# Performance work log

Measured on AMD Instinct MI355X. Metric: run time of the kernel, lower is better.

The kernel has to match this reference:

```python
import jax, jax.numpy as jnp
import numpy as np

N = 50000   # nodes
E = 800000  # edges (avg degree 16)
D = 128     # emb_dim
K = 3       # message passing rounds


def setup_inputs() -> dict:
    key = jax.random.key(0)
    ks = jax.random.split(key, 24)
    scale = jnp.float32(0.1)  # keep k iterated MLP magnitudes sane

    def w(k, shape):
        return jax.random.normal(k, shape, dtype=jnp.float32) * scale

    inp = {
        "feat": jax.random.normal(ks[0], (N, D), dtype=jnp.float32),
        "src": jax.random.randint(ks[1], (E,), 0, N, dtype=jnp.int32),
        "dst": jax.random.randint(ks[2], (E,), 0, N, dtype=jnp.int32),
    }
    i = 3
    for name in ["nt", "fp", "fu", "bp", "bu"]:
        inp[name + "_w1"] = w(ks[i], (D, D))
        inp[name + "_b1"] = w(ks[i + 1], (D,))
        inp[name + "_w2"] = w(ks[i + 2], (D, D))
        inp[name + "_b2"] = w(ks[i + 3], (D,))
        i += 4
    return inp


def _fnn(x, w1, b1, w2, b2):
    # FNN(in,[hid],out): Linear -> ReLU -> Linear (no final activation)
    return jnp.maximum(x @ w1 + b1, 0.0) @ w2 + b2


def _aggregate(y, src, dst, pw1, pb1, pw2, pb2, uw1, ub1, uw2, ub2):
    # gather src node states -> edge MLP (+ReLU) -> scatter-sum -> node MLP (+ReLU)
    msg = jnp.maximum(_fnn(y[src], pw1, pb1, pw2, pb2), 0.0)   # [E, D]
    z = jax.ops.segment_sum(msg, dst, num_segments=N)          # [N, D]
    return jnp.maximum(_fnn(z, uw1, ub1, uw2, ub2), 0.0)       # [N, D]


def _message_pass(self_trans, src, dst, sink, params):
    y = self_trans
    for _ in range(K):
        h = _aggregate(y, src, dst, *params)
        h = h.at[sink].set(0.0)  # zero the sink node row
        y = self_trans + h
    return y


def reference(feat, src, dst,
              nt_w1, nt_b1, nt_w2, nt_b2,
              fp_w1, fp_b1, fp_w2, fp_b2,
              fu_w1, fu_b1, fu_w2, fu_b2,
              bp_w1, bp_b1, bp_w2, bp_b2,
              bu_w1, bu_b1, bu_w2, bu_b2):
    self_trans = _fnn(feat, nt_w1, nt_b1, nt_w2, nt_b2)  # [N, D]
    # forward-direction aggregator, sink = last node
    out_fpa = _message_pass(self_trans, src, dst, N - 1,
                            (fp_w1, fp_b1, fp_w2, fp_b2,
                             fu_w1, fu_b1, fu_w2, fu_b2))
    # reversed graph (dgl.reverse swaps src/dst), sink = node 0
    out_bpa = _message_pass(self_trans, dst, src, 0,
                            (bp_w1, bp_b1, bp_w2, bp_b2,
                             bu_w1, bu_b1, bu_w2, bu_b2))
    return jnp.concatenate([out_fpa, out_bpa], axis=1)  # [N, 2D]
```

## Files before the change

### kernel.cpp

```cpp
#include <hip/hip_runtime.h>

#define Nn 50000
#define Ee 800000
#define Dd 128
#define Kk 3
#define TE 64
#define NT 256

#define LSTR 136
#define WSLOT 32768

#define NBUK 196
#define SCH 2048
#define SB ((Ee + SCH - 1) / SCH)

typedef short sh8 __attribute__((ext_vector_type(8)));
typedef float f32x4 __attribute__((ext_vector_type(4)));

__device__ __forceinline__ ushort bfsplit(float x, float* rem) {
  const unsigned u = __float_as_uint(x);
  *rem = x - __uint_as_float(u & 0xffff0000u);
  return (ushort)(u >> 16);
}
__device__ __forceinline__ ushort bftrunc(float x) {
  return (ushort)(__float_as_uint(x) >> 16);
}
__device__ __forceinline__ ushort f32_to_bf16_rtn(float x) {
  const unsigned u = __float_as_uint(x);
  return (ushort)((u + 0x7fffu + ((u >> 16) & 1u)) >> 16);
}

__device__ __forceinline__ void acc8(const uint4 v, float4& a0, float4& a1) {
  a0.x += __uint_as_float(v.x << 16);
  a0.y += __uint_as_float(v.x & 0xffff0000u);
  a0.z += __uint_as_float(v.y << 16);
  a0.w += __uint_as_float(v.y & 0xffff0000u);
  a1.x += __uint_as_float(v.z << 16);
  a1.y += __uint_as_float(v.z & 0xffff0000u);
  a1.z += __uint_as_float(v.w << 16);
  a1.w += __uint_as_float(v.w & 0xffff0000u);
}

#define MFMA_LAYER(WH, WL)                                                     \
  {                                                                            \
    _Pragma("unroll")                                                          \
    for (int c = 0; c < 4; ++c) {                                              \
      const sh8 bh0 = *(const sh8*)((WH) + (((nt0    ) * 4 + c) * 64 + lane) * 8); \
      const sh8 bh1 = *(const sh8*)((WH) + (((nt0 + 1) * 4 + c) * 64 + lane) * 8); \
      const sh8 bl0 = *(const sh8*)((WL) + (((nt0    ) * 4 + c) * 64 + lane) * 8); \
      const sh8 bl1 = *(const sh8*)((WL) + (((nt0 + 1) * 4 + c) * 64 + lane) * 8); \
      _Pragma("unroll")                                                        \
      for (int mt = 0; mt < 4; ++mt) {                                         \
        const int aoff = (mt * 16 + l15) * LSTR + c * 32 + q8 * 8;             \
        const sh8 ah = *(const sh8*)(Sh + aoff);                               \
        const sh8 al = *(const sh8*)(Sl + aoff);                               \
        acc[mt][0] = __builtin_amdgcn_mfma_f32_16x16x32_bf16(ah, bh0, acc[mt][0], 0, 0, 0); \
        acc[mt][1] = __builtin_amdgcn_mfma_f32_16x16x32_bf16(ah, bh1, acc[mt][1], 0, 0, 0); \
        acc[mt][0] = __builtin_amdgcn_mfma_f32_16x16x32_bf16(al, bh0, acc[mt][0], 0, 0, 0); \
        acc[mt][1] = __builtin_amdgcn_mfma_f32_16x16x32_bf16(al, bh1, acc[mt][1], 0, 0, 0); \
        acc[mt][0] = __builtin_amdgcn_mfma_f32_16x16x32_bf16(ah, bl0, acc[mt][0], 0, 0, 0); \
        acc[mt][1] = __builtin_amdgcn_mfma_f32_16x16x32_bf16(ah, bl1, acc[mt][1], 0, 0, 0); \
      }                                                                        \
    }                                                                          \
  }

#define ZERO_ACC                                                 \
  {                                                              \
    _Pragma("unroll")                                            \
    for (int mt = 0; mt < 4; ++mt)                               \
      _Pragma("unroll")                                          \
      for (int nl = 0; nl < 2; ++nl) {                           \
        acc[mt][nl][0] = 0.f; acc[mt][nl][1] = 0.f;              \
        acc[mt][nl][2] = 0.f; acc[mt][nl][3] = 0.f;              \
      }                                                          \
  }

#define HIDDEN_TO_LDS(B1ptr)                                     \
  {                                                              \
    const float b1a = (B1ptr)[w32 + l15];                        \
    const float b1b = (B1ptr)[w32 + 16 + l15];                   \
    _Pragma("unroll")                                            \
    for (int mt = 0; mt < 4; ++mt)                               \
      _Pragma("unroll")                                          \
      for (int nl = 0; nl < 2; ++nl) {                           \
        const int col = w32 + nl * 16 + l15;                     \
        const float bb = nl ? b1b : b1a;                         \
        _Pragma("unroll")                                        \
        for (int rg = 0; rg < 4; ++rg) {                         \
          const int row = mt * 16 + q8 * 4 + rg;                 \
          const float h = fmaxf(acc[mt][nl][rg] + bb, 0.f);      \
          float rm;                                              \
          const ushort hh = bfsplit(h, &rm);                     \
          const int off = row * LSTR + col;                      \
          Sh[off] = hh;                                          \
          Sl[off] = bftrunc(rm);                                 \
        }                                                        \
      }                                                          \
  }

#define STC_TO_LDS                                               \
  {                                                              \
    _Pragma("unroll")                                            \
    for (int mt = 0; mt < 4; ++mt)                               \
      _Pragma("unroll")                                          \
      for (int nl = 0; nl < 2; ++nl) {                           \
        const int col = w32 + nl * 16 + l15;                     \
        _Pragma("unroll")                                        \
        for (int rg = 0; rg < 4; ++rg) {                         \
          const int row = mt * 16 + q8 * 4 + rg;                 \
          float rm;                                              \
          const ushort hh = bfsplit(stc[mt][nl][rg], &rm);       \
          const int off = row * LSTR + col;                      \
          Sh[off] = hh;                                          \
          Sl[off] = bftrunc(rm);                                 \
        }                                                        \
      }                                                          \
  }

#define STAGE_ROWS(Xptr)                                                       \
  {                                                                            \
    _Pragma("unroll")                                                          \
    for (int it = 0; it < (TE * 32 / NT); ++it) {                              \
      const int i = t + NT * it;                                               \
      const int r = i >> 5;                                                    \
      const int c4 = (i & 31) << 2;                                            \
      float4 v = make_float4(0.f, 0.f, 0.f, 0.f);                              \
      if (r < nrow) v = *(const float4*)((Xptr) + (size_t)(row0 + r) * Dd + c4); \
      ushort4 hv, lv; float rm;                                                \
      hv.x = bfsplit(v.x, &rm); lv.x = bftrunc(rm);                            \
      hv.y = bfsplit(v.y, &rm); lv.y = bftrunc(rm);                            \
      hv.z = bfsplit(v.z, &rm); lv.z = bftrunc(rm);                            \
      hv.w = bfsplit(v.w, &rm); lv.w = bftrunc(rm);                            \
      *(ushort4*)(&Sh[r * LSTR + c4]) = hv;                                    \
      *(ushort4*)(&Sl[r * LSTR + c4]) = lv;                                    \
    }                                                                          \
  }

#define MFMA_PRELUDE                                             \
  const int lane = t & 63;                                       \
  const int wave = t >> 6;                                       \
  const int l15 = lane & 15;                                     \
  const int q8 = lane >> 4;                                      \
  const int w32 = wave * 32;                                     \
  const int nt0 = wave * 2;                                      \
  f32x4 acc[4][2];

struct DirP {
  const ushort *u1, *u2, *p1, *p2;
  const float *ub1, *ub2, *pb1, *pb2;
};

__global__ __launch_bounds__(NT) void stmsg_kernel(
    const float* __restrict__ X,
    const ushort* __restrict__ Wn1, const ushort* __restrict__ Wn2,
    const float* __restrict__ Bn1, const float* __restrict__ Bn2,
    DirP pf, DirP pb,
    float* __restrict__ st, ushort* __restrict__ Mf, ushort* __restrict__ Mb)
{
  __shared__ __align__(16) ushort Sbuf[2 * TE * LSTR];
  ushort* Sh = Sbuf;
  ushort* Sl = Sbuf + TE * LSTR;
  const int t = threadIdx.x;
  const int row0 = blockIdx.x * TE;
  const int rem = Nn - row0;
  const int nrow = rem < TE ? rem : TE;

  STAGE_ROWS(X);
  __syncthreads();
  MFMA_PRELUDE;

  ZERO_ACC;
  MFMA_LAYER(Wn1, Wn1 + 16384);
  __syncthreads();
  HIDDEN_TO_LDS(Bn1);
  __syncthreads();
  ZERO_ACC;
  MFMA_LAYER(Wn2, Wn2 + 16384);

  float stc[4][2][4];
  {
    const float b2a = Bn2[w32 + l15];
    const float b2b = Bn2[w32 + 16 + l15];
    #pragma unroll
    for (int mt = 0; mt < 4; ++mt)
      #pragma unroll
      for (int nl = 0; nl < 2; ++nl) {
        const int col = w32 + nl * 16 + l15;
        const float bb = nl ? b2b : b2a;
        #pragma unroll
        for (int rg = 0; rg < 4; ++rg) {
          const int row = mt * 16 + q8 * 4 + rg;
          const float v = acc[mt][nl][rg] + bb;
          stc[mt][nl][rg] = v;
          if (row < nrow) st[(size_t)(row0 + row) * Dd + col] = v;
        }
      }
  }
  __syncthreads();

  STC_TO_LDS;
  __syncthreads();
  ZERO_ACC;
  MFMA_LAYER(pf.p1, pf.p1 + 16384);
  __syncthreads();
  HIDDEN_TO_LDS(pf.pb1);
  __syncthreads();
  ZERO_ACC;
  MFMA_LAYER(pf.p2, pf.p2 + 16384);
  {
    const float b2a = pf.pb2[w32 + l15];
    const float b2b = pf.pb2[w32 + 16 + l15];
    #pragma unroll
    for (int mt = 0; mt < 4; ++mt)
      #pragma unroll
      for (int nl = 0; nl < 2; ++nl) {
        const int col = w32 + nl * 16 + l15;
        const float bb = nl ? b2b : b2a;
        #pragma unroll
        for (int rg = 0; rg < 4; ++rg) {
          const int row = mt * 16 + q8 * 4 + rg;
          if (row < nrow)
            Mf[(size_t)(row0 + row) * Dd + col] =
                f32_to_bf16_rtn(fmaxf(acc[mt][nl][rg] + bb, 0.f));
        }
      }
  }
  __syncthreads();

  STC_TO_LDS;
  __syncthreads();
  ZERO_ACC;
  MFMA_LAYER(pb.p1, pb.p1 + 16384);
  __syncthreads();
  HIDDEN_TO_LDS(pb.pb1);
  __syncthreads();
  ZERO_ACC;
  MFMA_LAYER(pb.p2, pb.p2 + 16384);
  {
    const float b2a = pb.pb2[w32 + l15];
    const float b2b = pb.pb2[w32 + 16 + l15];
    #pragma unroll
    for (int mt = 0; mt < 4; ++mt)
      #pragma unroll
      for (int nl = 0; nl < 2; ++nl) {
        const int col = w32 + nl * 16 + l15;
        const float bb = nl ? b2b : b2a;
        #pragma unroll
        for (int rg = 0; rg < 4; ++rg) {
          const int row = mt * 16 + q8 * 4 + rg;
          if (row < nrow)
            Mb[(size_t)(row0 + row) * Dd + col] =
                f32_to_bf16_rtn(fmaxf(acc[mt][nl][rg] + bb, 0.f));
        }
      }
  }
}

template <int DO_MSG>
__global__ __launch_bounds__(NT) void aggupdmsg_kernel(
    const ushort* __restrict__ Min_f, const ushort* __restrict__ Min_b,
    const int* __restrict__ rp_f, const int* __restrict__ rp_b,
    const int* __restrict__ col_f, const int* __restrict__ col_b,
    const float* __restrict__ st,
    ushort* __restrict__ RMf, ushort* __restrict__ RMb,
    float* __restrict__ RYf, float* __restrict__ RYb, int rstride,
    DirP pf, DirP pb, int nhalf)
{
  __shared__ __align__(16) ushort Sbuf[2 * TE * LSTR];
  ushort* Sh = Sbuf;
  ushort* Sl = Sbuf + TE * LSTR;
  const int t = threadIdx.x;
  const int dir = blockIdx.x >= nhalf;
  const int row0 = (blockIdx.x - dir * nhalf) * TE;
  const int rem = Nn - row0;
  const int nrow = rem < TE ? rem : TE;
  const DirP P = dir ? pb : pf;
  const ushort* Min = dir ? Min_b : Min_f;
  const int* rp = dir ? rp_b : rp_f;
  const int* col = dir ? col_b : col_f;
  ushort* RoutM = dir ? RMb : RMf;
  float* RoutY = dir ? RYb : RYf;
  const int sink = dir ? 0 : (Nn - 1);

  {
    const int nr = t >> 2;
    const int q4 = t & 3;
    const int qb = (t & 63) & 60;
    float4 za[8];
    #pragma unroll
    for (int i = 0; i < 8; ++i) za[i] = make_float4(0.f, 0.f, 0.f, 0.f);
    if (nr < nrow) {
      const int gnode = row0 + nr;
      int e = rp[gnode];
      const int ee = rp[gnode + 1];
      const ushort* Mq4 = Min + q4 * 8;
      for (; e + 3 < ee; e += 4) {
        const int cm = col[e + q4];
        const int c0 = __shfl(cm, qb);
        const int c1 = __shfl(cm, qb + 1);
        const int c2 = __shfl(cm, qb + 2);
        const int c3 = __shfl(cm, qb + 3);
        const ushort* r0 = Mq4 + (size_t)c0 * Dd;
        const ushort* r1 = Mq4 + (size_t)c1 * Dd;
        const ushort* r2 = Mq4 + (size_t)c2 * Dd;
        const ushort* r3 = Mq4 + (size_t)c3 * Dd;
        uint4 v0[4], v1[4], v2[4], v3[4];
        #pragma unroll
        for (int i = 0; i < 4; ++i) v0[i] = *(const uint4*)(r0 + i * 32);
        #pragma unroll
        for (int i = 0; i < 4; ++i) v1[i] = *(const uint4*)(r1 + i * 32);
        #pragma unroll
        for (int i = 0; i < 4; ++i) v2[i] = *(const uint4*)(r2 + i * 32);
        #pragma unroll
        for (int i = 0; i < 4; ++i) v3[i] = *(const uint4*)(r3 + i * 32);
        #pragma unroll
        for (int i = 0; i < 4; ++i) {
          acc8(v0[i], za[2 * i], za[2 * i + 1]);
          acc8(v1[i], za[2 * i], za[2 * i + 1]);
          acc8(v2[i], za[2 * i], za[2 * i + 1]);
          acc8(v3[i], za[2 * i], za[2 * i + 1]);
        }
      }
      for (; e < ee; ++e) {
        const ushort* r0 = Mq4 + (size_t)col[e] * Dd;
        #pragma unroll
        for (int i = 0; i < 4; ++i)
          acc8(*(const uint4*)(r0 + i * 32), za[2 * i], za[2 * i + 1]);
      }
    }
    #pragma unroll
    for (int k = 0; k < 8; ++k) {
      ushort4 hv, lv; float rm;
      hv.x = bfsplit(za[k].x, &rm); lv.x = bftrunc(rm);
      hv.y = bfsplit(za[k].y, &rm); lv.y = bftrunc(rm);
      hv.z = bfsplit(za[k].z, &rm); lv.z = bftrunc(rm);
      hv.w = bfsplit(za[k].w, &rm); lv.w = bftrunc(rm);
      const int c4 = (k >> 1) * 32 + q4 * 8 + (k & 1) * 4;
      *(ushort4*)(&Sh[nr * LSTR + c4]) = hv;
      *(ushort4*)(&Sl[nr * LSTR + c4]) = lv;
    }
  }
  __syncthreads();

  MFMA_PRELUDE;

  ZERO_ACC;
  MFMA_LAYER(P.u1, P.u1 + 16384);
  __syncthreads();
  HIDDEN_TO_LDS(P.ub1);
  __syncthreads();
  ZERO_ACC;
  MFMA_LAYER(P.u2, P.u2 + 16384);

  {
    const float b2a = P.ub2[w32 + l15];
    const float b2b = P.ub2[w32 + 16 + l15];
    if (DO_MSG) __syncthreads();
    #pragma unroll
    for (int mt = 0; mt < 4; ++mt)
      #pragma unroll
      for (int nl = 0; nl < 2; ++nl) {
        const int col = w32 + nl * 16 + l15;
        const float bb = nl ? b2b : b2a;
        #pragma unroll
        for (int rg = 0; rg < 4; ++rg) {
          const int row = mt * 16 + q8 * 4 + rg;
          float v = 0.f;
          if (row < nrow) {
            const int gr = row0 + row;
            v = fmaxf(acc[mt][nl][rg] + bb, 0.f);
            if (gr == sink) v = 0.f;
            v += st[(size_t)gr * Dd + col];
          }
          if (DO_MSG) {
            float rm;
            const ushort hh = bfsplit(v, &rm);
            const int off = row * LSTR + col;
            Sh[off] = hh;
            Sl[off] = bftrunc(rm);
          } else if (row < nrow) {
            RoutY[(size_t)(row0 + row) * rstride + col] = v;
          }
        }
      }
  }

  if (DO_MSG) {
    __syncthreads();
    ZERO_ACC;
    MFMA_LAYER(P.p1, P.p1 + 16384);
    __syncthreads();
    HIDDEN_TO_LDS(P.pb1);
    __syncthreads();
    ZERO_ACC;
    MFMA_LAYER(P.p2, P.p2 + 16384);

    const float b2a = P.pb2[w32 + l15];
    const float b2b = P.pb2[w32 + 16 + l15];
    #pragma unroll
    for (int mt = 0; mt < 4; ++mt)
      #pragma unroll
      for (int nl = 0; nl < 2; ++nl) {
        const int col = w32 + nl * 16 + l15;
        const float bb = nl ? b2b : b2a;
        #pragma unroll
        for (int rg = 0; rg < 4; ++rg) {
          const int row = mt * 16 + q8 * 4 + rg;
          if (row < nrow)
            RoutM[(size_t)(row0 + row) * Dd + col] =
                f32_to_bf16_rtn(fmaxf(acc[mt][nl][rg] + bb, 0.f));
        }
      }
  }
}

struct WPtrs { const float* w[10]; };

__global__ void pack_w_kernel(WPtrs P, ushort* __restrict__ out)
{
  const int id = blockIdx.x * blockDim.x + threadIdx.x;
  const int mat = blockIdx.y;
  const int j = id & 7;
  const int lane = (id >> 3) & 63;
  const int ch = (id >> 9) & 3;
  const int nt = id >> 11;
  const int k = ch * 32 + (lane >> 4) * 8 + j;
  const int n = nt * 16 + (lane & 15);
  const float x = P.w[mat][k * Dd + n];
  float rm;
  const ushort h = bfsplit(x, &rm);
  out[(size_t)mat * WSLOT + id] = h;
  out[(size_t)mat * WSLOT + 16384 + id] = bftrunc(rm);
}

__global__ __launch_bounds__(256) void csr_count(
    const int* __restrict__ src, const int* __restrict__ dst,
    int* __restrict__ bcnt)
{
  const int dirv = blockIdx.y;
  const int* key = dirv ? src : dst;
  __shared__ int h[NBUK];
  const int t = threadIdx.x;
  if (t < NBUK) h[t] = 0;
  __syncthreads();
  const int e0 = blockIdx.x * SCH;
  #pragma unroll
  for (int i = 0; i < SCH / 256; ++i) {
    const int e = e0 + i * 256 + t;
    if (e < Ee) atomicAdd(&h[key[e] >> 8], 1);
  }
  __syncthreads();
  if (t < NBUK && h[t] > 0) atomicAdd(&bcnt[dirv * 256 + t], h[t]);
}

__global__ __launch_bounds__(256) void csr_scan(
    const int* __restrict__ bcnt, int* __restrict__ bbase,
    int* __restrict__ bcur, int* __restrict__ rp)
{
  __shared__ int s[256];
  const int t = threadIdx.x;
  for (int y = 0; y < 2; ++y) {
    const int v = (t < NBUK) ? bcnt[y * 256 + t] : 0;
    s[t] = v;
    __syncthreads();
    for (int off = 1; off < 256; off <<= 1) {
      int x = s[t];
      if (t >= off) x += s[t - off];
      __syncthreads();
      s[t] = x;
      __syncthreads();
    }
    const int excl = s[t] - v;
    if (t < NBUK) { bbase[y * 257 + t] = excl; bcur[y * 256 + t] = excl; }
    if (t == NBUK - 1) bbase[y * 257 + NBUK] = s[t];
    if (t == 0) rp[y * (Nn + 1) + Nn] = Ee;
    __syncthreads();
  }
}

__global__ __launch_bounds__(256) void csr_scatter(
    const int* __restrict__ src, const int* __restrict__ dst,
    int* __restrict__ bcur, uint* __restrict__ pairs)
{
  const int dirv = blockIdx.y;
  const int* key = dirv ? src : dst;
  const int* val = dirv ? dst : src;
  __shared__ int lh[NBUK], gb[NBUK], lc[NBUK];
  const int t = threadIdx.x;
  if (t < NBUK) { lh[t] = 0; lc[t] = 0; }
  __syncthreads();
  const int e0 = blockIdx.x * SCH;
  int ks[SCH / 256], vs[SCH / 256];
  #pragma unroll
  for (int i = 0; i < SCH / 256; ++i) {
    const int e = e0 + i * 256 + t;
    ks[i] = (e < Ee) ? key[e] : -1;
    vs[i] = (e < Ee) ? val[e] : 0;
    if (ks[i] >= 0) atomicAdd(&lh[ks[i] >> 8], 1);
  }
  __syncthreads();
  if (t < NBUK && lh[t] > 0) gb[t] = atomicAdd(&bcur[dirv * 256 + t], lh[t]);
  __syncthreads();
  uint* pd = pairs + (size_t)dirv * Ee;
  #pragma unroll
  for (int i = 0; i < SCH / 256; ++i) {
    if (ks[i] >= 0) {
      const int b = ks[i] >> 8;
      const int r = atomicAdd(&lc[b], 1);
      pd[gb[b] + r] = ((uint)ks[i] << 16) | (uint)vs[i];
    }
  }
}

__global__ __launch_bounds__(256) void csr_final(
    const uint* __restrict__ pairs, const int* __restrict__ bbase,
    int* __restrict__ rp, int* __restrict__ col_f, int* __restrict__ col_b)
{
  const int dirv = blockIdx.y;
  const int b = blockIdx.x;
  const int base = bbase[dirv * 257 + b];
  const int cnt = bbase[dirv * 257 + b + 1] - base;
  const uint* pd = pairs + (size_t)dirv * Ee + base;
  int* colo = dirv ? col_b : col_f;
  __shared__ int h[256];
  __shared__ int s[256];
  const int t = threadIdx.x;
  h[t] = 0;
  __syncthreads();
  for (int i = t; i < cnt; i += 256) atomicAdd(&h[(pd[i] >> 16) & 255], 1);
  __syncthreads();
  const int v = h[t];
  s[t] = v;
  __syncthreads();
  for (int off = 1; off < 256; off <<= 1) {
    int x = s[t];
    if (t >= off) x += s[t - off];
    __syncthreads();
    s[t] = x;
    __syncthreads();
  }
  const int excl = s[t] - v;
  const int node = b * 256 + t;
  if (node < Nn) rp[dirv * (Nn + 1) + node] = base + excl;
  h[t] = excl;
  __syncthreads();
  for (int i = t; i < cnt; i += 256) {
    const uint p = pd[i];
    const int k = (p >> 16) & 255;
    const int r = atomicAdd(&h[k], 1);
    colo[base + r] = (int)(p & 0xffffu);
  }
}

extern "C" void kernel_launch(void* const* d_in, const int* in_sizes, int n_in,
                              void* d_out, int out_size, void* d_ws, size_t ws_size,
                              hipStream_t stream)
{
  const float* feat = (const float*)d_in[0];
  const int*   src  = (const int*)d_in[1];
  const int*   dst  = (const int*)d_in[2];

  const float* W[5][4];
  for (int p = 0; p < 5; ++p)
    for (int q = 0; q < 4; ++q)
      W[p][q] = (const float*)d_in[3 + p * 4 + q];

  float* st = (float*)d_ws;
  ushort* Mp_f = (ushort*)(st + (size_t)Nn * Dd);
  ushort* Mp_b = Mp_f + (size_t)Nn * Dd;
  ushort* Mq_f = Mp_b + (size_t)Nn * Dd;
  ushort* Mq_b = Mq_f + (size_t)Nn * Dd;
  int* ip       = (int*)(Mq_b + (size_t)Nn * Dd);
  int* rp_f     = ip;                 ip += Nn + 1;
  int* rp_b     = ip;                 ip += Nn + 1;
  int* col_f    = ip;                 ip += Ee;
  int* col_b    = ip;                 ip += Ee;
  int* bcnt     = ip;                 ip += 2 * 256;
  int* bbase    = ip;                 ip += 2 * 257;
  int* bcur     = ip;                 ip += 2 * 256;
  ushort* Wp = (ushort*)(((uintptr_t)ip + 63) & ~(uintptr_t)63);
  float* out = (float*)d_out;

  uint* pairs = (uint*)Mq_f;

  const int nodeBlocks = (Nn + TE - 1) / TE;
  const int dualBlocks = 2 * nodeBlocks;

  WPtrs wpk;
  for (int p = 0; p < 5; ++p) { wpk.w[2 * p] = W[p][0]; wpk.w[2 * p + 1] = W[p][2]; }
  pack_w_kernel<<<dim3(64, 10), NT, 0, stream>>>(wpk, Wp);

  hipMemsetAsync(bcnt, 0, 2 * 256 * sizeof(int), stream);
  csr_count<<<dim3(SB, 2), 256, 0, stream>>>(src, dst, bcnt);
  csr_scan<<<1, 256, 0, stream>>>(bcnt, bbase, bcur, rp_f);
  csr_scatter<<<dim3(SB, 2), 256, 0, stream>>>(src, dst, bcur, pairs);
  csr_final<<<dim3(NBUK, 2), 256, 0, stream>>>(pairs, bbase, rp_f, col_f, col_b);

  #define WS(m) (Wp + (size_t)(m) * WSLOT)
  DirP Pf = { WS(4), WS(5), WS(2), WS(3), W[2][1], W[2][3], W[1][1], W[1][3] };
  DirP Pb = { WS(8), WS(9), WS(6), WS(7), W[4][1], W[4][3], W[3][1], W[3][3] };

  stmsg_kernel<<<nodeBlocks, NT, 0, stream>>>(
      feat, WS(0), WS(1), W[0][1], W[0][3], Pf, Pb, st, Mp_f, Mp_b);

  aggupdmsg_kernel<1><<<dualBlocks, NT, 0, stream>>>(
      Mp_f, Mp_b, rp_f, rp_b, col_f, col_b, st,
      Mq_f, Mq_b, nullptr, nullptr, 0, Pf, Pb, nodeBlocks);

  aggupdmsg_kernel<1><<<dualBlocks, NT, 0, stream>>>(
      Mq_f, Mq_b, rp_f, rp_b, col_f, col_b, st,
      Mp_f, Mp_b, nullptr, nullptr, 0, Pf, Pb, nodeBlocks);

  aggupdmsg_kernel<0><<<dualBlocks, NT, 0, stream>>>(
      Mp_f, Mp_b, rp_f, rp_b, col_f, col_b, st,
      nullptr, nullptr, out, out + Dd, 2 * Dd, Pf, Pb, nodeBlocks);

  #undef WS
}
```

Baseline: 582.8 us.

## Double block threads to 512, one 16-col MFMA tile per wave, 8-lane gather

Raises the thread count per block from 256 to 512, so each of 8 waves computes one 16-column output tile in the MFMA layers instead of two, halving per-wave accumulator registers. The neighbor gather is reorganized so 8 lanes cooperate per node, each loading 16 bytes from two halves of a row, and 8 edges are unrolled per iteration instead of 4. This aims at more memory-level parallelism and occupancy for the gather-bound aggregation. In exchange, each block carries more waves across its syncs, and the A-tile LDS reads are now repeated by more waves.

```diff
diff --git a/kernel.cpp b/kernel.cpp
--- a/kernel.cpp
+++ b/kernel.cpp
@@ -6,6 +6,7 @@
 #define Kk 3
 #define TE 64
 #define NT 256
+#define NTM 512
 
 #define LSTR 136
 #define WSLOT 32768
@@ -45,21 +46,16 @@
   {                                                                            \
     _Pragma("unroll")                                                          \
     for (int c = 0; c < 4; ++c) {                                              \
-      const sh8 bh0 = *(const sh8*)((WH) + (((nt0    ) * 4 + c) * 64 + lane) * 8); \
-      const sh8 bh1 = *(const sh8*)((WH) + (((nt0 + 1) * 4 + c) * 64 + lane) * 8); \
-      const sh8 bl0 = *(const sh8*)((WL) + (((nt0    ) * 4 + c) * 64 + lane) * 8); \
-      const sh8 bl1 = *(const sh8*)((WL) + (((nt0 + 1) * 4 + c) * 64 + lane) * 8); \
+      const sh8 bh = *(const sh8*)((WH) + ((wave * 4 + c) * 64 + lane) * 8);   \
+      const sh8 bl = *(const sh8*)((WL) + ((wave * 4 + c) * 64 + lane) * 8);   \
       _Pragma("unroll")                                                        \
       for (int mt = 0; mt < 4; ++mt) {                                         \
         const int aoff = (mt * 16 + l15) * LSTR + c * 32 + q8 * 8;             \
         const sh8 ah = *(const sh8*)(Sh + aoff);                               \
         const sh8 al = *(const sh8*)(Sl + aoff);                               \
-        acc[mt][0] = __builtin_amdgcn_mfma_f32_16x16x32_bf16(ah, bh0, acc[mt][0], 0, 0, 0); \
-        acc[mt][1] = __builtin_amdgcn_mfma_f32_16x16x32_bf16(ah, bh1, acc[mt][1], 0, 0, 0); \
-        acc[mt][0] = __builtin_amdgcn_mfma_f32_16x16x32_bf16(al, bh0, acc[mt][0], 0, 0, 0); \
-        acc[mt][1] = __builtin_amdgcn_mfma_f32_16x16x32_bf16(al, bh1, acc[mt][1], 0, 0, 0); \
-        acc[mt][0] = __builtin_amdgcn_mfma_f32_16x16x32_bf16(ah, bl0, acc[mt][0], 0, 0, 0); \
-        acc[mt][1] = __builtin_amdgcn_mfma_f32_16x16x32_bf16(ah, bl1, acc[mt][1], 0, 0, 0); \
+        acc[mt] = __builtin_amdgcn_mfma_f32_16x16x32_bf16(ah, bh, acc[mt], 0, 0, 0); \
+        acc[mt] = __builtin_amdgcn_mfma_f32_16x16x32_bf16(al, bh, acc[mt], 0, 0, 0); \
+        acc[mt] = __builtin_amdgcn_mfma_f32_16x16x32_bf16(ah, bl, acc[mt], 0, 0, 0); \
       }                                                                        \
     }                                                                          \
   }
@@ -67,34 +63,26 @@
 #define ZERO_ACC                                                 \
   {                                                              \
     _Pragma("unroll")                                            \
-    for (int mt = 0; mt < 4; ++mt)                               \
-      _Pragma("unroll")                                          \
-      for (int nl = 0; nl < 2; ++nl) {                           \
-        acc[mt][nl][0] = 0.f; acc[mt][nl][1] = 0.f;              \
-        acc[mt][nl][2] = 0.f; acc[mt][nl][3] = 0.f;              \
-      }                                                          \
+    for (int mt = 0; mt < 4; ++mt) {                             \
+      acc[mt][0] = 0.f; acc[mt][1] = 0.f;                        \
+      acc[mt][2] = 0.f; acc[mt][3] = 0.f;                        \
+    }                                                            \
   }
 
 #define HIDDEN_TO_LDS(B1ptr)                                     \
   {                                                              \
-    const float b1a = (B1ptr)[w32 + l15];                        \
-    const float b1b = (B1ptr)[w32 + 16 + l15];                   \
+    const float bb = (B1ptr)[w16 + l15];                         \
     _Pragma("unroll")                                            \
     for (int mt = 0; mt < 4; ++mt)                               \
       _Pragma("unroll")                                          \
-      for (int nl = 0; nl < 2; ++nl) {                           \
-        const int col = w32 + nl * 16 + l15;                     \
-        const float bb = nl ? b1b : b1a;                         \
-        _Pragma("unroll")                                        \
-        for (int rg = 0; rg < 4; ++rg) {                         \
-          const int row = mt * 16 + q8 * 4 + rg;                 \
-          const float h = fmaxf(acc[mt][nl][rg] + bb, 0.f);      \
-          float rm;                                              \
-          const ushort hh = bfsplit(h, &rm);                     \
-          const int off = row * LSTR + col;                      \
-          Sh[off] = hh;                                          \
-          Sl[off] = bftrunc(rm);                                 \
-        }                                                        \
+      for (int rg = 0; rg < 4; ++rg) {                           \
+        const int row = mt * 16 + q8 * 4 + rg;                   \
+        const float h = fmaxf(acc[mt][rg] + bb, 0.f);            \
+        float rm;                                                \
+        const ushort hh = bfsplit(h, &rm);                       \
+        const int off = row * LSTR + w16 + l15;                  \
+        Sh[off] = hh;                                            \
+        Sl[off] = bftrunc(rm);                                   \
       }                                                          \
   }
 
@@ -103,25 +91,21 @@
     _Pragma("unroll")                                            \
     for (int mt = 0; mt < 4; ++mt)                               \
       _Pragma("unroll")                                          \
-      for (int nl = 0; nl < 2; ++nl) {                           \
-        const int col = w32 + nl * 16 + l15;                     \
-        _Pragma("unroll")                                        \
-        for (int rg = 0; rg < 4; ++rg) {                         \
-          const int row = mt * 16 + q8 * 4 + rg;                 \
-          float rm;                                              \
-          const ushort hh = bfsplit(stc[mt][nl][rg], &rm);       \
-          const int off = row * LSTR + col;                      \
-          Sh[off] = hh;                                          \
-          Sl[off] = bftrunc(rm);                                 \
-        }                                                        \
+      for (int rg = 0; rg < 4; ++rg) {                           \
+        const int row = mt * 16 + q8 * 4 + rg;                   \
+        float rm;                                                \
+        const ushort hh = bfsplit(stc[mt][rg], &rm);             \
+        const int off = row * LSTR + w16 + l15;                  \
+        Sh[off] = hh;                                            \
+        Sl[off] = bftrunc(rm);                                   \
       }                                                          \
   }
 
 #define STAGE_ROWS(Xptr)                                                       \
   {                                                                            \
     _Pragma("unroll")                                                          \
-    for (int it = 0; it < (TE * 32 / NT); ++it) {                              \
-      const int i = t + NT * it;                                               \
+    for (int it = 0; it < (TE * 32 / NTM); ++it) {                             \
+      const int i = t + NTM * it;                                              \
       const int r = i >> 5;                                                    \
       const int c4 = (i & 31) << 2;                                            \
       float4 v = make_float4(0.f, 0.f, 0.f, 0.f);                              \
@@ -141,16 +125,15 @@
   const int wave = t >> 6;                                       \
   const int l15 = lane & 15;                                     \
   const int q8 = lane >> 4;                                      \
-  const int w32 = wave * 32;                                     \
-  const int nt0 = wave * 2;                                      \
-  f32x4 acc[4][2];
+  const int w16 = wave * 16;                                     \
+  f32x4 acc[4];
 
 struct DirP {
   const ushort *u1, *u2, *p1, *p2;
   const float *ub1, *ub2, *pb1, *pb2;
 };
 
-__global__ __launch_bounds__(NT) void stmsg_kernel(
+__global__ __launch_bounds__(NTM) void stmsg_kernel(
     const float* __restrict__ X,
     const ushort* __restrict__ Wn1, const ushort* __restrict__ Wn2,
     const float* __restrict__ Bn1, const float* __restrict__ Bn2,
@@ -177,23 +160,17 @@
   ZERO_ACC;
   MFMA_LAYER(Wn2, Wn2 + 16384);
 
-  float stc[4][2][4];
+  float stc[4][4];
   {
-    const float b2a = Bn2[w32 + l15];
-    const float b2b = Bn2[w32 + 16 + l15];
+    const float b2 = Bn2[w16 + l15];
     #pragma unroll
     for (int mt = 0; mt < 4; ++mt)
       #pragma unroll
-      for (int nl = 0; nl < 2; ++nl) {
-        const int col = w32 + nl * 16 + l15;
-        const float bb = nl ? b2b : b2a;
-        #pragma unroll
-        for (int rg = 0; rg < 4; ++rg) {
-          const int row = mt * 16 + q8 * 4 + rg;
-          const float v = acc[mt][nl][rg] + bb;
-          stc[mt][nl][rg] = v;
-          if (row < nrow) st[(size_t)(row0 + row) * Dd + col] = v;
-        }
+      for (int rg = 0; rg < 4; ++rg) {
+        const int row = mt * 16 + q8 * 4 + rg;
+        const float v = acc[mt][rg] + b2;
+        stc[mt][rg] = v;
+        if (row < nrow) st[(size_t)(row0 + row) * Dd + w16 + l15] = v;
       }
   }
   __syncthreads();
@@ -208,21 +185,15 @@
   ZERO_ACC;
   MFMA_LAYER(pf.p2, pf.p2 + 16384);
   {
-    const float b2a = pf.pb2[w32 + l15];
-    const float b2b = pf.pb2[w32 + 16 + l15];
+    const float b2 = pf.pb2[w16 + l15];
     #pragma unroll
     for (int mt = 0; mt < 4; ++mt)
       #pragma unroll
-      for (int nl = 0; nl < 2; ++nl) {
-        const int col = w32 + nl * 16 + l15;
-        const float bb = nl ? b2b : b2a;
-        #pragma unroll
-        for (int rg = 0; rg < 4; ++rg) {
-          const int row = mt * 16 + q8 * 4 + rg;
-          if (row < nrow)
-            Mf[(size_t)(row0 + row) * Dd + col] =
-                f32_to_bf16_rtn(fmaxf(acc[mt][nl][rg] + bb, 0.f));
-        }
+      for (int rg = 0; rg < 4; ++rg) {
+        const int row = mt * 16 + q8 * 4 + rg;
+        if (row < nrow)
+          Mf[(size_t)(row0 + row) * Dd + w16 + l15] =
+              f32_to_bf16_rtn(fmaxf(acc[mt][rg] + b2, 0.f));
       }
   }
   __syncthreads();
@@ -237,27 +208,21 @@
   ZERO_ACC;
   MFMA_LAYER(pb.p2, pb.p2 + 16384);
   {
-    const float b2a = pb.pb2[w32 + l15];
-    const float b2b = pb.pb2[w32 + 16 + l15];
+    const float b2 = pb.pb2[w16 + l15];
     #pragma unroll
     for (int mt = 0; mt < 4; ++mt)
       #pragma unroll
-      for (int nl = 0; nl < 2; ++nl) {
-        const int col = w32 + nl * 16 + l15;
-        const float bb = nl ? b2b : b2a;
-        #pragma unroll
-        for (int rg = 0; rg < 4; ++rg) {
-          const int row = mt * 16 + q8 * 4 + rg;
-          if (row < nrow)
-            Mb[(size_t)(row0 + row) * Dd + col] =
-                f32_to_bf16_rtn(fmaxf(acc[mt][nl][rg] + bb, 0.f));
-        }
+      for (int rg = 0; rg < 4; ++rg) {
+        const int row = mt * 16 + q8 * 4 + rg;
+        if (row < nrow)
+          Mb[(size_t)(row0 + row) * Dd + w16 + l15] =
+              f32_to_bf16_rtn(fmaxf(acc[mt][rg] + b2, 0.f));
       }
   }
 }
 
 template <int DO_MSG>
-__global__ __launch_bounds__(NT) void aggupdmsg_kernel(
+__global__ __launch_bounds__(NTM) void aggupdmsg_kernel(
     const ushort* __restrict__ Min_f, const ushort* __restrict__ Min_b,
     const int* __restrict__ rp_f, const int* __restrict__ rp_b,
     const int* __restrict__ col_f, const int* __restrict__ col_b,
@@ -283,59 +248,47 @@
   const int sink = dir ? 0 : (Nn - 1);
 
   {
-    const int nr = t >> 2;
-    const int q4 = t & 3;
-    const int qb = (t & 63) & 60;
-    float4 za[8];
-    #pragma unroll
-    for (int i = 0; i < 8; ++i) za[i] = make_float4(0.f, 0.f, 0.f, 0.f);
+    const int nr = t >> 3;
+    const int o8 = t & 7;
+    const int ob = (t & 63) & ~7;
+    float4 za[4];
+    #pragma unroll
+    for (int i = 0; i < 4; ++i) za[i] = make_float4(0.f, 0.f, 0.f, 0.f);
     if (nr < nrow) {
       const int gnode = row0 + nr;
       int e = rp[gnode];
       const int ee = rp[gnode + 1];
-      const ushort* Mq4 = Min + q4 * 8;
-      for (; e + 3 < ee; e += 4) {
-        const int cm = col[e + q4];
-        const int c0 = __shfl(cm, qb);
-        const int c1 = __shfl(cm, qb + 1);
-        const int c2 = __shfl(cm, qb + 2);
-        const int c3 = __shfl(cm, qb + 3);
-        const ushort* r0 = Mq4 + (size_t)c0 * Dd;
-        const ushort* r1 = Mq4 + (size_t)c1 * Dd;
-        const ushort* r2 = Mq4 + (size_t)c2 * Dd;
-        const ushort* r3 = Mq4 + (size_t)c3 * Dd;
-        uint4 v0[4], v1[4], v2[4], v3[4];
+      const ushort* Mo = Min + o8 * 8;
+      for (; e + 7 < ee; e += 8) {
+        const int cm = col[e + o8];
+        uint4 va[8], vb[8];
         #pragma unroll
-        for (int i = 0; i < 4; ++i) v0[i] = *(const uint4*)(r0 + i * 32);
+        for (int k = 0; k < 8; ++k) {
+          const int ck = __shfl(cm, ob + k);
+          const ushort* rk = Mo + (size_t)ck * Dd;
+          va[k] = *(const uint4*)(rk);
+          vb[k] = *(const uint4*)(rk + 64);
+        }
         #pragma unroll
-        for (int i = 0; i < 4; ++i) v1[i] = *(const uint4*)(r1 + i * 32);
-        #pragma unroll
-        for (int i = 0; i < 4; ++i) v2[i] = *(const uint4*)(r2 + i * 32);
-        #pragma unroll
-        for (int i = 0; i < 4; ++i) v3[i] = *(const uint4*)(r3 + i * 32);
-        #pragma unroll
-        for (int i = 0; i < 4; ++i) {
-          acc8(v0[i], za[2 * i], za[2 * i + 1]);
-          acc8(v1[i], za[2 * i], za[2 * i + 1]);
-          acc8(v2[i], za[2 * i], za[2 * i + 1]);
-          acc8(v3[i], za[2 * i], za[2 * i + 1]);
+        for (int k = 0; k < 8; ++k) {
+          acc8(va[k], za[0], za[1]);
+          acc8(vb[k], za[2], za[3]);
         }
       }
       for (; e < ee; ++e) {
-        const ushort* r0 = Mq4 + (size_t)col[e] * Dd;
-        #pragma unroll
-        for (int i = 0; i < 4; ++i)
-          acc8(*(const uint4*)(r0 + i * 32), za[2 * i], za[2 * i + 1]);
+        const ushort* rk = Mo + (size_t)col[e] * Dd;
+        acc8(*(const uint4*)(rk), za[0], za[1]);
+        acc8(*(const uint4*)(rk + 64), za[2], za[3]);
       }
     }
     #pragma unroll
-    for (int k = 0; k < 8; ++k) {
+    for (int k = 0; k < 4; ++k) {
       ushort4 hv, lv; float rm;
       hv.x = bfsplit(za[k].x, &rm); lv.x = bftrunc(rm);
       hv.y = bfsplit(za[k].y, &rm); lv.y = bftrunc(rm);
       hv.z = bfsplit(za[k].z, &rm); lv.z = bftrunc(rm);
       hv.w = bfsplit(za[k].w, &rm); lv.w = bftrunc(rm);
-      const int c4 = (k >> 1) * 32 + q4 * 8 + (k & 1) * 4;
+      const int c4 = (k >> 1) * 64 + o8 * 8 + (k & 1) * 4;
       *(ushort4*)(&Sh[nr * LSTR + c4]) = hv;
       *(ushort4*)(&Sl[nr * LSTR + c4]) = lv;
     }
@@ -353,34 +306,28 @@
   MFMA_LAYER(P.u2, P.u2 + 16384);
 
   {
-    const float b2a = P.ub2[w32 + l15];
-    const float b2b = P.ub2[w32 + 16 + l15];
+    const float b2 = P.ub2[w16 + l15];
     if (DO_MSG) __syncthreads();
     #pragma unroll
     for (int mt = 0; mt < 4; ++mt)
       #pragma unroll
-      for (int nl = 0; nl < 2; ++nl) {
-        const int col = w32 + nl * 16 + l15;
-        const float bb = nl ? b2b : b2a;
-        #pragma unroll
-        for (int rg = 0; rg < 4; ++rg) {
-          const int row = mt * 16 + q8 * 4 + rg;
-          float v = 0.f;
-          if (row < nrow) {
-            const int gr = row0 + row;
-            v = fmaxf(acc[mt][nl][rg] + bb, 0.f);
-            if (gr == sink) v = 0.f;
-            v += st[(size_t)gr * Dd + col];
-          }
-          if (DO_MSG) {
-            float rm;
-            const ushort hh = bfsplit(v, &rm);
-            const int off = row * LSTR + col;
-            Sh[off] = hh;
-            Sl[off] = bftrunc(rm);
-          } else if (row < nrow) {
-            RoutY[(size_t)(row0 + row) * rstride + col] = v;
-          }
+      for (int rg = 0; rg < 4; ++rg) {
+        const int row = mt * 16 + q8 * 4 + rg;
+        float v = 0.f;
+        if (row < nrow) {
+          const int gr = row0 + row;
+          v = fmaxf(acc[mt][rg] + b2, 0.f);
+          if (gr == sink) v = 0.f;
+          v += st[(size_t)gr * Dd + w16 + l15];
+        }
+        if (DO_MSG) {
+          float rm;
+          const ushort hh = bfsplit(v, &rm);
+          const int off = row * LSTR + w16 + l15;
+          Sh[off] = hh;
+          Sl[off] = bftrunc(rm);
+        } else if (row < nrow) {
+          RoutY[(size_t)(row0 + row) * rstride + w16 + l15] = v;
         }
       }
   }
@@ -395,21 +342,15 @@
     ZERO_ACC;
     MFMA_LAYER(P.p2, P.p2 + 16384);
 
-    const float b2a = P.pb2[w32 + l15];
-    const float b2b = P.pb2[w32 + 16 + l15];
+    const float b2 = P.pb2[w16 + l15];
     #pragma unroll
     for (int mt = 0; mt < 4; ++mt)
       #pragma unroll
-      for (int nl = 0; nl < 2; ++nl) {
-        const int col = w32 + nl * 16 + l15;
-        const float bb = nl ? b2b : b2a;
-        #pragma unroll
-        for (int rg = 0; rg < 4; ++rg) {
-          const int row = mt * 16 + q8 * 4 + rg;
-          if (row < nrow)
-            RoutM[(size_t)(row0 + row) * Dd + col] =
-                f32_to_bf16_rtn(fmaxf(acc[mt][nl][rg] + bb, 0.f));
-        }
+      for (int rg = 0; rg < 4; ++rg) {
+        const int row = mt * 16 + q8 * 4 + rg;
+        if (row < nrow)
+          RoutM[(size_t)(row0 + row) * Dd + w16 + l15] =
+              f32_to_bf16_rtn(fmaxf(acc[mt][rg] + b2, 0.f));
       }
   }
 }
@@ -600,18 +541,18 @@
   DirP Pf = { WS(4), WS(5), WS(2), WS(3), W[2][1], W[2][3], W[1][1], W[1][3] };
   DirP Pb = { WS(8), WS(9), WS(6), WS(7), W[4][1], W[4][3], W[3][1], W[3][3] };
 
-  stmsg_kernel<<<nodeBlocks, NT, 0, stream>>>(
+  stmsg_kernel<<<nodeBlocks, NTM, 0, stream>>>(
       feat, WS(0), WS(1), W[0][1], W[0][3], Pf, Pb, st, Mp_f, Mp_b);
 
-  aggupdmsg_kernel<1><<<dualBlocks, NT, 0, stream>>>(
+  aggupdmsg_kernel<1><<<dualBlocks, NTM, 0, stream>>>(
       Mp_f, Mp_b, rp_f, rp_b, col_f, col_b, st,
       Mq_f, Mq_b, nullptr, nullptr, 0, Pf, Pb, nodeBlocks);
 
-  aggupdmsg_kernel<1><<<dualBlocks, NT, 0, stream>>>(
+  aggupdmsg_kernel<1><<<dualBlocks, NTM, 0, stream>>>(
       Mq_f, Mq_b, rp_f, rp_b, col_f, col_b, st,
       Mp_f, Mp_b, nullptr, nullptr, 0, Pf, Pb, nodeBlocks);
 
-  aggupdmsg_kernel<0><<<dualBlocks, NT, 0, stream>>>(
+  aggupdmsg_kernel<0><<<dualBlocks, NTM, 0, stream>>>(
       Mp_f, Mp_b, rp_f, rp_b, col_f, col_b, st,
       nullptr, nullptr, out, out + Dd, 2 * Dd, Pf, Pb, nodeBlocks);
 
```

After: 713.8 us. 1.22x slower.

## Halve aggregation tile, widen per-node gather threads, sort CSR columns by source band

Applied to the files above, without the earlier changes.

The aggregate/update/message kernel now processes 32 nodes per block instead of 64. Each node gets 8 threads, each owning 16 contiguous features, replacing the previous 4-thread shuffle scheme. This doubles the grid and shrinks LDS use, aiming at better occupancy and load balance for the gather-bound phase, at the cost of reloading the MLP weights in twice as many blocks. Separately, the CSR finalize kernel caches bucket pairs in LDS and writes each node's column list ordered by source-index band, for better gather locality in later rounds, with extra passes and shared memory added to that kernel.

```diff
diff --git a/kernel.cpp b/kernel.cpp
--- a/kernel.cpp
+++ b/kernel.cpp
@@ -5,6 +5,7 @@
 #define Dd 128
 #define Kk 3
 #define TE 64
+#define TEA 32
 #define NT 256
 
 #define LSTR 136
@@ -13,6 +14,7 @@
 #define NBUK 196
 #define SCH 2048
 #define SB ((Ee + SCH - 1) / SCH)
+#define FCAP 5632
 
 typedef short sh8 __attribute__((ext_vector_type(8)));
 typedef float f32x4 __attribute__((ext_vector_type(4)));
@@ -41,7 +43,7 @@
   a1.w += __uint_as_float(v.w & 0xffff0000u);
 }
 
-#define MFMA_LAYER(WH, WL)                                                     \
+#define MFMA_LAYER(WH, WL, MT)                                                 \
   {                                                                            \
     _Pragma("unroll")                                                          \
     for (int c = 0; c < 4; ++c) {                                              \
@@ -50,7 +52,7 @@
       const sh8 bl0 = *(const sh8*)((WL) + (((nt0    ) * 4 + c) * 64 + lane) * 8); \
       const sh8 bl1 = *(const sh8*)((WL) + (((nt0 + 1) * 4 + c) * 64 + lane) * 8); \
       _Pragma("unroll")                                                        \
-      for (int mt = 0; mt < 4; ++mt) {                                         \
+      for (int mt = 0; mt < (MT); ++mt) {                                      \
         const int aoff = (mt * 16 + l15) * LSTR + c * 32 + q8 * 8;             \
         const sh8 ah = *(const sh8*)(Sh + aoff);                               \
         const sh8 al = *(const sh8*)(Sl + aoff);                               \
@@ -64,10 +66,10 @@
     }                                                                          \
   }
 
-#define ZERO_ACC                                                 \
+#define ZERO_ACC(MT)                                             \
   {                                                              \
     _Pragma("unroll")                                            \
-    for (int mt = 0; mt < 4; ++mt)                               \
+    for (int mt = 0; mt < (MT); ++mt)                            \
       _Pragma("unroll")                                          \
       for (int nl = 0; nl < 2; ++nl) {                           \
         acc[mt][nl][0] = 0.f; acc[mt][nl][1] = 0.f;              \
@@ -75,12 +77,12 @@
       }                                                          \
   }
 
-#define HIDDEN_TO_LDS(B1ptr)                                     \
+#define HIDDEN_TO_LDS(B1ptr, MT)                                 \
   {                                                              \
     const float b1a = (B1ptr)[w32 + l15];                        \
     const float b1b = (B1ptr)[w32 + 16 + l15];                   \
     _Pragma("unroll")                                            \
-    for (int mt = 0; mt < 4; ++mt)                               \
+    for (int mt = 0; mt < (MT); ++mt)                            \
       _Pragma("unroll")                                          \
       for (int nl = 0; nl < 2; ++nl) {                           \
         const int col = w32 + nl * 16 + l15;                     \
@@ -98,10 +100,10 @@
       }                                                          \
   }
 
-#define STC_TO_LDS                                               \
+#define STC_TO_LDS(MT)                                           \
   {                                                              \
     _Pragma("unroll")                                            \
-    for (int mt = 0; mt < 4; ++mt)                               \
+    for (int mt = 0; mt < (MT); ++mt)                            \
       _Pragma("unroll")                                          \
       for (int nl = 0; nl < 2; ++nl) {                           \
         const int col = w32 + nl * 16 + l15;                     \
@@ -136,14 +138,14 @@
     }                                                                          \
   }
 
-#define MFMA_PRELUDE                                             \
+#define MFMA_PRELUDE(MT)                                         \
   const int lane = t & 63;                                       \
   const int wave = t >> 6;                                       \
   const int l15 = lane & 15;                                     \
   const int q8 = lane >> 4;                                      \
   const int w32 = wave * 32;                                     \
   const int nt0 = wave * 2;                                      \
-  f32x4 acc[4][2];
+  f32x4 acc[MT][2];
 
 struct DirP {
   const ushort *u1, *u2, *p1, *p2;
@@ -167,15 +169,15 @@
 
   STAGE_ROWS(X);
   __syncthreads();
-  MFMA_PRELUDE;
-
-  ZERO_ACC;
-  MFMA_LAYER(Wn1, Wn1 + 16384);
-  __syncthreads();
-  HIDDEN_TO_LDS(Bn1);
-  __syncthreads();
-  ZERO_ACC;
-  MFMA_LAYER(Wn2, Wn2 + 16384);
+  MFMA_PRELUDE(4);
+
+  ZERO_ACC(4);
+  MFMA_LAYER(Wn1, Wn1 + 16384, 4);
+  __syncthreads();
+  HIDDEN_TO_LDS(Bn1, 4);
+  __syncthreads();
+  ZERO_ACC(4);
+  MFMA_LAYER(Wn2, Wn2 + 16384, 4);
 
   float stc[4][2][4];
   {
@@ -198,15 +200,15 @@
   }
   __syncthreads();
 
-  STC_TO_LDS;
-  __syncthreads();
-  ZERO_ACC;
-  MFMA_LAYER(pf.p1, pf.p1 + 16384);
-  __syncthreads();
-  HIDDEN_TO_LDS(pf.pb1);
-  __syncthreads();
-  ZERO_ACC;
-  MFMA_LAYER(pf.p2, pf.p2 + 16384);
+  STC_TO_LDS(4);
+  __syncthreads();
+  ZERO_ACC(4);
+  MFMA_LAYER(pf.p1, pf.p1 + 16384, 4);
+  __syncthreads();
+  HIDDEN_TO_LDS(pf.pb1, 4);
+  __syncthreads();
+  ZERO_ACC(4);
+  MFMA_LAYER(pf.p2, pf.p2 + 16384, 4);
   {
     const float b2a = pf.pb2[w32 + l15];
     const float b2b = pf.pb2[w32 + 16 + l15];
@@ -227,15 +229,15 @@
   }
   __syncthreads();
 
-  STC_TO_LDS;
-  __syncthreads();
-  ZERO_ACC;
-  MFMA_LAYER(pb.p1, pb.p1 + 16384);
-  __syncthreads();
-  HIDDEN_TO_LDS(pb.pb1);
-  __syncthreads();
-  ZERO_ACC;
-  MFMA_LAYER(pb.p2, pb.p2 + 16384);
+  STC_TO_LDS(4);
+  __syncthreads();
+  ZERO_ACC(4);
+  MFMA_LAYER(pb.p1, pb.p1 + 16384, 4);
+  __syncthreads();
+  HIDDEN_TO_LDS(pb.pb1, 4);
+  __syncthreads();
+  ZERO_ACC(4);
+  MFMA_LAYER(pb.p2, pb.p2 + 16384, 4);
   {
     const float b2a = pb.pb2[w32 + l15];
     const float b2b = pb.pb2[w32 + 16 + l15];
@@ -266,14 +268,14 @@
     float* __restrict__ RYf, float* __restrict__ RYb, int rstride,
     DirP pf, DirP pb, int nhalf)
 {
-  __shared__ __align__(16) ushort Sbuf[2 * TE * LSTR];
+  __shared__ __align__(16) ushort Sbuf[2 * TEA * LSTR];
   ushort* Sh = Sbuf;
-  ushort* Sl = Sbuf + TE * LSTR;
+  ushort* Sl = Sbuf + TEA * LSTR;
   const int t = threadIdx.x;
   const int dir = blockIdx.x >= nhalf;
-  const int row0 = (blockIdx.x - dir * nhalf) * TE;
+  const int row0 = (blockIdx.x - dir * nhalf) * TEA;
   const int rem = Nn - row0;
-  const int nrow = rem < TE ? rem : TE;
+  const int nrow = rem < TEA ? rem : TEA;
   const DirP P = dir ? pb : pf;
   const ushort* Min = dir ? Min_b : Min_f;
   const int* rp = dir ? rp_b : rp_f;
@@ -283,81 +285,70 @@
   const int sink = dir ? 0 : (Nn - 1);
 
   {
-    const int nr = t >> 2;
-    const int q4 = t & 3;
-    const int qb = (t & 63) & 60;
-    float4 za[8];
+    const int nr = t >> 3;
+    const int o8 = t & 7;
+    float4 za[4];
     #pragma unroll
-    for (int i = 0; i < 8; ++i) za[i] = make_float4(0.f, 0.f, 0.f, 0.f);
+    for (int i = 0; i < 4; ++i) za[i] = make_float4(0.f, 0.f, 0.f, 0.f);
     if (nr < nrow) {
       const int gnode = row0 + nr;
       int e = rp[gnode];
       const int ee = rp[gnode + 1];
-      const ushort* Mq4 = Min + q4 * 8;
+      const ushort* Mo = Min + o8 * 16;
       for (; e + 3 < ee; e += 4) {
-        const int cm = col[e + q4];
-        const int c0 = __shfl(cm, qb);
-        const int c1 = __shfl(cm, qb + 1);
-        const int c2 = __shfl(cm, qb + 2);
-        const int c3 = __shfl(cm, qb + 3);
-        const ushort* r0 = Mq4 + (size_t)c0 * Dd;
-        const ushort* r1 = Mq4 + (size_t)c1 * Dd;
-        const ushort* r2 = Mq4 + (size_t)c2 * Dd;
-        const ushort* r3 = Mq4 + (size_t)c3 * Dd;
-        uint4 v0[4], v1[4], v2[4], v3[4];
-        #pragma unroll
-        for (int i = 0; i < 4; ++i) v0[i] = *(const uint4*)(r0 + i * 32);
-        #pragma unroll
-        for (int i = 0; i < 4; ++i) v1[i] = *(const uint4*)(r1 + i * 32);
-        #pragma unroll
-        for (int i = 0; i < 4; ++i) v2[i] = *(const uint4*)(r2 + i * 32);
-        #pragma unroll
-        for (int i = 0; i < 4; ++i) v3[i] = *(const uint4*)(r3 + i * 32);
-        #pragma unroll
-        for (int i = 0; i < 4; ++i) {
-          acc8(v0[i], za[2 * i], za[2 * i + 1]);
-          acc8(v1[i], za[2 * i], za[2 * i + 1]);
-          acc8(v2[i], za[2 * i], za[2 * i + 1]);
-          acc8(v3[i], za[2 * i], za[2 * i + 1]);
-        }
+        const int c0 = col[e];
+        const int c1 = col[e + 1];
+        const int c2 = col[e + 2];
+        const int c3 = col[e + 3];
+        const ushort* r0 = Mo + (size_t)c0 * Dd;
+        const ushort* r1 = Mo + (size_t)c1 * Dd;
+        const ushort* r2 = Mo + (size_t)c2 * Dd;
+        const ushort* r3 = Mo + (size_t)c3 * Dd;
+        uint4 a0 = *(const uint4*)(r0), b0 = *(const uint4*)(r0 + 8);
+        uint4 a1 = *(const uint4*)(r1), b1 = *(const uint4*)(r1 + 8);
+        uint4 a2 = *(const uint4*)(r2), b2 = *(const uint4*)(r2 + 8);
+        uint4 a3 = *(const uint4*)(r3), b3 = *(const uint4*)(r3 + 8);
+        acc8(a0, za[0], za[1]); acc8(b0, za[2], za[3]);
+        acc8(a1, za[0], za[1]); acc8(b1, za[2], za[3]);
+        acc8(a2, za[0], za[1]); acc8(b2, za[2], za[3]);
+        acc8(a3, za[0], za[1]); acc8(b3, za[2], za[3]);
       }
       for (; e < ee; ++e) {
-        const ushort* r0 = Mq4 + (size_t)col[e] * Dd;
-        #pragma unroll
-        for (int i = 0; i < 4; ++i)
-          acc8(*(const uint4*)(r0 + i * 32), za[2 * i], za[2 * i + 1]);
+        const ushort* r0 = Mo + (size_t)col[e] * Dd;
+        acc8(*(const uint4*)(r0), za[0], za[1]);
+        acc8(*(const uint4*)(r0 + 8), za[2], za[3]);
       }
     }
     #pragma unroll
-    for (int k = 0; k < 8; ++k) {
+    for (int k = 0; k < 4; ++k) {
       ushort4 hv, lv; float rm;
       hv.x = bfsplit(za[k].x, &rm); lv.x = bftrunc(rm);
       hv.y = bfsplit(za[k].y, &rm); lv.y = bftrunc(rm);
       hv.z = bfsplit(za[k].z, &rm); lv.z = bftrunc(rm);
       hv.w = bfsplit(za[k].w, &rm); lv.w = bftrunc(rm);
-      const int c4 = (k >> 1) * 32 + q4 * 8 + (k & 1) * 4;
+      const int c4 = o8 * 16 + k * 4;
       *(ushort4*)(&Sh[nr * LSTR + c4]) = hv;
       *(ushort4*)(&Sl[nr * LSTR + c4]) = lv;
     }
   }
   __syncthreads();
 
-  MFMA_PRELUDE;
-
-  ZERO_ACC;
-  MFMA_LAYER(P.u1, P.u1 + 16384);
-  __syncthreads();
-  HIDDEN_TO_LDS(P.ub1);
-  __syncthreads();
-  ZERO_ACC;
-  MFMA_LAYER(P.u2, P.u2 + 16384);
+  MFMA_PRELUDE(2);
+
+  ZERO_ACC(2);
+  MFMA_LAYER(P.u1, P.u1 + 16384, 2);
+  __syncthreads();
+  HIDDEN_TO_LDS(P.ub1, 2);
+  __syncthreads();
+  ZERO_ACC(2);
+  MFMA_LAYER(P.u2, P.u2 + 16384, 2);
 
   {
     const float b2a = P.ub2[w32 + l15];
     const float b2b = P.ub2[w32 + 16 + l15];
     if (DO_MSG) __syncthreads();
     #pragma unroll
-    for (int mt = 0; mt < 4; ++mt)
+    for (int mt = 0; mt < 2; ++mt)
       #pragma unroll
       for (int nl = 0; nl < 2; ++nl) {
         const int col = w32 + nl * 16 + l15;
@@ -387,18 +378,18 @@
 
   if (DO_MSG) {
     __syncthreads();
-    ZERO_ACC;
-    MFMA_LAYER(P.p1, P.p1 + 16384);
+    ZERO_ACC(2);
+    MFMA_LAYER(P.p1, P.p1 + 16384, 2);
     __syncthreads();
-    HIDDEN_TO_LDS(P.pb1);
+    HIDDEN_TO_LDS(P.pb1, 2);
     __syncthreads();
-    ZERO_ACC;
-    MFMA_LAYER(P.p2, P.p2 + 16384);
+    ZERO_ACC(2);
+    MFMA_LAYER(P.p2, P.p2 + 16384, 2);
 
     const float b2a = P.pb2[w32 + l15];
     const float b2b = P.pb2[w32 + 16 + l15];
     #pragma unroll
-    for (int mt = 0; mt < 4; ++mt)
+    for (int mt = 0; mt < 2; ++mt)
       #pragma unroll
       for (int nl = 0; nl < 2; ++nl) {
         const int col = w32 + nl * 16 + l15;
@@ -524,10 +515,21 @@
   int* colo = dirv ? col_b : col_f;
   __shared__ int h[256];
   __shared__ int s[256];
+  __shared__ uint pr[FCAP];
+  __shared__ int cols[FCAP];
   const int t = threadIdx.x;
   h[t] = 0;
   __syncthreads();
-  for (int i = t; i < cnt; i += 256) atomicAdd(&h[(pd[i] >> 16) & 255], 1);
+  const bool fits = (cnt <= FCAP);
+  if (fits) {
+    for (int i = t; i < cnt; i += 256) {
+      const uint p = pd[i];
+      pr[i] = p;
+      atomicAdd(&h[(p >> 16) & 255], 1);
+    }
+  } else {
+    for (int i = t; i < cnt; i += 256) atomicAdd(&h[(pd[i] >> 16) & 255], 1);
+  }
   __syncthreads();
   const int v = h[t];
   s[t] = v;
@@ -544,11 +546,27 @@
   if (node < Nn) rp[dirv * (Nn + 1) + node] = base + excl;
   h[t] = excl;
   __syncthreads();
-  for (int i = t; i < cnt; i += 256) {
-    const uint p = pd[i];
-    const int k = (p >> 16) & 255;
-    const int r = atomicAdd(&h[k], 1);
-    colo[base + r] = (int)(p & 0xffffu);
+  if (fits) {
+    for (int band = 0; band < 8; ++band) {
+      for (int i = t; i < cnt; i += 256) {
+        const uint p = pr[i];
+        const int vv = (int)(p & 0xffffu);
+        if ((vv >> 13) == band) {
+          const int k = (p >> 16) & 255;
+          const int r = atomicAdd(&h[k], 1);
+          cols[r] = vv;
+        }
+      }
+      __syncthreads();
+    }
+    for (int i = t; i < cnt; i += 256) colo[base + i] = cols[i];
+  } else {
+    for (int i = t; i < cnt; i += 256) {
+      const uint p = pd[i];
+      const int k = (p >> 16) & 255;
+      const int r = atomicAdd(&h[k], 1);
+      colo[base + r] = (int)(p & 0xffffu);
+    }
   }
 }
 
@@ -584,7 +602,8 @@
   uint* pairs = (uint*)Mq_f;
 
   const int nodeBlocks = (Nn + TE - 1) / TE;
-  const int dualBlocks = 2 * nodeBlocks;
+  const int aggBlocks  = (Nn + TEA - 1) / TEA;
+  const int dualBlocks = 2 * aggBlocks;
 
   WPtrs wpk;
   for (int p = 0; p < 5; ++p) { wpk.w[2 * p] = W[p][0]; wpk.w[2 * p + 1] = W[p][2]; }
@@ -605,15 +624,15 @@
 
   aggupdmsg_kernel<1><<<dualBlocks, NT, 0, stream>>>(
       Mp_f, Mp_b, rp_f, rp_b, col_f, col_b, st,
-      Mq_f, Mq_b, nullptr, nullptr, 0, Pf, Pb, nodeBlocks);
+      Mq_f, Mq_b, nullptr, nullptr, 0, Pf, Pb, aggBlocks);
 
   aggupdmsg_kernel<1><<<dualBlocks, NT, 0, stream>>>(
       Mq_f, Mq_b, rp_f, rp_b, col_f, col_b, st,
-      Mp_f, Mp_b, nullptr, nullptr, 0, Pf, Pb, nodeBlocks);
+      Mp_f, Mp_b, nullptr, nullptr, 0, Pf, Pb, aggBlocks);
 
   aggupdmsg_kernel<0><<<dualBlocks, NT, 0, stream>>>(
       Mp_f, Mp_b, rp_f, rp_b, col_f, col_b, st,
-      nullptr, nullptr, out, out + Dd, 2 * Dd, Pf, Pb, nodeBlocks);
+      nullptr, nullptr, out, out + Dd, 2 * Dd, Pf, Pb, aggBlocks);
 
   #undef WS
 }
```

Measured after the change: 544.9 us. 6.5% less time.
